# Kernel optimization log

Measured on AMD Instinct MI355X. Metric: run time of the kernel, lower is better.

## Reference

```python
import jax, jax.numpy as jnp
import numpy as np
import math

TOP_K = 2
CAP_FACTOR = 1.25
AUX_W = 0.01


def setup_inputs() -> dict:
    key = jax.random.key(0)
    k1, k2 = jax.random.split(key)
    x = jax.random.normal(k1, (8192, 4096), dtype=jnp.float32)
    # gate weight, torch init std=0.01, stored as (E, D) like nn.Linear
    gate_w = jax.random.normal(k2, (64, 4096), dtype=jnp.float32) * 0.01
    return {"x": x, "gate_w": gate_w}


def reference(x, gate_w):
    N, D = x.shape
    E = gate_w.shape[0]
    K = TOP_K
    C = max(math.ceil(CAP_FACTOR * N / E), 1)  # expert capacity

    logits = x @ gate_w.T                      # (N, E)
    probs = jax.nn.softmax(logits, axis=-1)    # (N, E)
    vals, idx = jax.lax.top_k(probs, K)        # (N, K)
    vals = vals / vals.sum(axis=-1, keepdims=True)

    # Parallel replacement of the serial double loop: flatten (N,K) row-major
    # (token-major, then k) which matches the loop iteration order exactly.
    flat_e = idx.reshape(-1)                               # (N*K,) expert ids
    oh = jax.nn.one_hot(flat_e, E, dtype=jnp.int32)        # (N*K, E)
    # exclusive prefix count of prior assignments to each expert
    pos = jnp.cumsum(oh, axis=0) - oh                      # (N*K, E)
    slot = jnp.take_along_axis(pos, flat_e[:, None], axis=1)[:, 0]  # (N*K,)
    # In the torch loop the counter saturates at C (only incremented when
    # c < C), so slot==prior_total is equivalent: kept iff prior_total < C.
    keep = slot < C
    slot_s = jnp.where(keep, slot, 0)
    tok = jnp.arange(N * K) // K

    combine_weights = jnp.zeros((N, E, C), dtype=x.dtype).at[
        tok, flat_e, slot_s].add(jnp.where(keep, vals.reshape(-1), 0.0))
    dispatch_mask = (jnp.zeros((N, E, C), dtype=jnp.int32).at[
        tok, flat_e, slot_s].add(keep.astype(jnp.int32))) > 0

    # load balancing loss
    f = oh.astype(jnp.float32).reshape(N, K, E).mean(axis=(0, 1))  # (E,)
    p = probs.mean(axis=0)                                         # (E,)
    load_loss = AUX_W * E * jnp.sum(f * p)

    return dispatch_mask, combine_weights, probs, load_loss
```

## Files before the change

### kernel.cpp

```cpp
#include <hip/hip_runtime.h>
#include <math.h>

#define N_TOK 8192
#define DIM   4096
#define NEXP  64
#define CAP   160
#define OFF_CW    (83886080ULL)
#define OFF_PROBS (167772160ULL)
#define OFF_LOSS  (168296448ULL)
#define NA    16384
#define SPLIT 8

typedef float vfloat4 __attribute__((ext_vector_type(4)));

__device__ __forceinline__ float wave_max64(float v) {
    for (int m = 1; m < 64; m <<= 1) v = fmaxf(v, __shfl_xor(v, m, 64));
    return v;
}
__device__ __forceinline__ float wave_sum64(float v) {
    for (int m = 1; m < 64; m <<= 1) v += __shfl_xor(v, m, 64);
    return v;
}
__device__ __forceinline__ void wave_argmax64(float& v, int& i) {
    for (int m = 1; m < 64; m <<= 1) {
        float ov = __shfl_xor(v, m, 64);
        int   oi = __shfl_xor(i, m, 64);
        if (ov > v || (ov == v && oi < i)) { v = ov; i = oi; }
    }
}

__global__ __launch_bounds__(256) void k_gemm_zero(const float* __restrict__ x,
                                                   const float* __restrict__ gw,
                                                   float* __restrict__ part,
                                                   float* __restrict__ out) {
    __shared__ float xs[64][68];
    __shared__ float wsh[64][68];
    const int tb = (blockIdx.x & 127) * 64;
    const int sy = blockIdx.x >> 7;
    const int d_begin = sy * (DIM / SPLIT);
    const int t  = threadIdx.x;
    const int tx = t & 15, ty = t >> 4;
    float* zbase = out + (size_t)blockIdx.x * 163840;
    const vfloat4 z = {0.f, 0.f, 0.f, 0.f};
    float acc[4][4] = {};
    for (int ci = 0; ci < (DIM / SPLIT) / 64; ++ci) {
        const int d0 = d_begin + ci * 64;
        for (int it = 0; it < 4; ++it) {
            int idx = t + 256 * it;
            int row = idx >> 4;
            int d4  = idx & 15;
            *(float4*)(&xs[row][4 * d4]) =
                *(const float4*)(x + (size_t)(tb + row) * DIM + d0 + 4 * d4);
            *(float4*)(&wsh[row][4 * d4]) =
                *(const float4*)(gw + (size_t)row * DIM + d0 + 4 * d4);
        }
        #pragma unroll
        for (int zi = 0; zi < 5; ++zi)
            __builtin_nontemporal_store(
                z, (vfloat4*)(zbase + 4 * ((ci * 5 + zi) * 256 + t)));
        __syncthreads();
        for (int d4 = 0; d4 < 16; ++d4) {
            float4 xa[4], wb[4];
            for (int i = 0; i < 4; ++i) xa[i] = *(const float4*)(&xs[ty + 16 * i][4 * d4]);
            for (int j = 0; j < 4; ++j) wb[j] = *(const float4*)(&wsh[tx + 16 * j][4 * d4]);
            for (int i = 0; i < 4; ++i)
                for (int j = 0; j < 4; ++j) {
                    acc[i][j] = fmaf(xa[i].x, wb[j].x, acc[i][j]);
                    acc[i][j] = fmaf(xa[i].y, wb[j].y, acc[i][j]);
                    acc[i][j] = fmaf(xa[i].z, wb[j].z, acc[i][j]);
                    acc[i][j] = fmaf(xa[i].w, wb[j].w, acc[i][j]);
                }
        }
        __syncthreads();
    }
    for (int i = 0; i < 4; ++i)
        for (int j = 0; j < 4; ++j)
            part[(size_t)sy * N_TOK * NEXP +
                 (size_t)(tb + ty + 16 * i) * NEXP + (tx + 16 * j)] = acc[i][j];
}

__global__ __launch_bounds__(256) void k_router(const float* __restrict__ part,
                                                float* __restrict__ probs_out,
                                                int* __restrict__ rec_e,
                                                float* __restrict__ rec_w) {
    const int tok  = blockIdx.x * 4 + (threadIdx.x >> 6);
    const int lane = threadIdx.x & 63;
    float l = 0.f;
    for (int s = 0; s < SPLIT; ++s)
        l += part[(size_t)s * N_TOK * NEXP + (size_t)tok * NEXP + lane];
    const float m  = wave_max64(l);
    const float ex = expf(l - m);
    const float sm = wave_sum64(ex);
    const float p  = ex / sm;
    probs_out[(size_t)tok * NEXP + lane] = p;
    float v1 = p; int i1 = lane;
    wave_argmax64(v1, i1);
    float v2 = (lane == i1) ? -1.f : p; int i2 = lane;
    wave_argmax64(v2, i2);
    if (lane == 0) {
        const float denom = v1 + v2;
        rec_e[2 * tok]     = i1;
        rec_e[2 * tok + 1] = i2;
        rec_w[2 * tok]     = v1 / denom;
        rec_w[2 * tok + 1] = v2 / denom;
    }
}

__global__ __launch_bounds__(256) void k_preduce(const float* __restrict__ probs,
                                                 float* __restrict__ psum_part) {
    __shared__ float sh[256];
    const int e = threadIdx.x & 63, tg = threadIdx.x >> 6;
    const int tok0 = blockIdx.x * 128;
    float a = 0.f;
    for (int k = 0; k < 32; ++k)
        a += probs[(size_t)(tok0 + tg + 4 * k) * NEXP + e];
    sh[threadIdx.x] = a;
    __syncthreads();
    if (threadIdx.x < 64)
        psum_part[blockIdx.x * 64 + threadIdx.x] =
            sh[threadIdx.x] + sh[64 + threadIdx.x] +
            sh[128 + threadIdx.x] + sh[192 + threadIdx.x];
}

__global__ __launch_bounds__(256) void k_assign_scatter(const int* __restrict__ rec_e,
                                                        const float* __restrict__ rec_w,
                                                        const float* __restrict__ psum_part,
                                                        float* __restrict__ out) {
    if (blockIdx.x == 16) {
        __shared__ int hcnt[64];
        if (threadIdx.x < 64) hcnt[threadIdx.x] = 0;
        __syncthreads();
        for (int j = 0; j < 64; ++j) {
            const int e = rec_e[j * 256 + threadIdx.x];
            atomicAdd(&hcnt[e], 1);
        }
        __syncthreads();
        if (threadIdx.x < 64) {
            const int e = threadIdx.x;
            float ps = 0.f;
            for (int b = 0; b < 64; ++b) ps += psum_part[b * 64 + e];
            float term = ((float)hcnt[e] / (float)NA) * (ps / (float)N_TOK);
            term = wave_sum64(term);
            if (e == 0) out[OFF_LOSS] = 0.01f * 64.f * term;
        }
        return;
    }
    const int w    = blockIdx.x * 4 + (threadIdx.x >> 6);
    const int lane = threadIdx.x & 63;
    int base = 0;
    const unsigned long long ltmask = (1ull << lane) - 1ull;
    #pragma unroll 4
    for (int c = 0; c < NA / 64; ++c) {
        const int i = c * 64 + lane;
        const int e = rec_e[i];
        const unsigned long long mask = __ballot(e == w);
        if (e == w) {
            const int slot = base + __popcll(mask & ltmask);
            if (slot < CAP) {
                const int tok = i >> 1;
                const size_t off = (size_t)tok * (NEXP * CAP) + (size_t)w * CAP + slot;
                out[off]          = 1.0f;
                out[OFF_CW + off] = rec_w[i];
            }
        }
        base += __popcll(mask);
    }
}

extern "C" void kernel_launch(void* const* d_in, const int* in_sizes, int n_in,
                              void* d_out, int out_size, void* d_ws, size_t ws_size,
                              hipStream_t stream) {
    const float* x  = (const float*)d_in[0];
    const float* gw = (const float*)d_in[1];
    float* out = (float*)d_out;

    char* w = (char*)d_ws;
    float* part      = (float*)w;
    int*   rec_e     = (int*)(w + (size_t)SPLIT * N_TOK * NEXP * 4);
    float* rec_w     = (float*)((char*)rec_e + NA * 4);
    float* psum_part = (float*)((char*)rec_w + NA * 4);

    k_gemm_zero<<<1024, 256, 0, stream>>>(x, gw, part, out);
    k_router<<<2048, 256, 0, stream>>>(part, out + OFF_PROBS, rec_e, rec_w);
    k_preduce<<<64, 256, 0, stream>>>(out + OFF_PROBS, psum_part);
    k_assign_scatter<<<17, 256, 0, stream>>>(rec_e, rec_w, psum_part, out);
}
```

Measured before the change: 763.2 us.

## Compute gate GEMM one token per lane with scalar-broadcast weights

Replaces the LDS-tiled 64x64 gate GEMM with a scheme where each lane owns one token and keeps 64 expert accumulators in registers. The weight slice is wave-uniform, so it can be read as broadcast/scalar loads. This removes shared memory staging and barriers. The grid shrinks from 1024 to 256 blocks, with each block zeroing four times as much output, so occupancy is lower and the per-lane x reads are strided across rows rather than coalesced. That could limit how well the dominant output zero-fill stores keep the memory system busy.

```diff
diff --git a/kernel.cpp b/kernel.cpp
--- a/kernel.cpp
+++ b/kernel.cpp
@@ -10,6 +10,9 @@
 #define OFF_LOSS  (168296448ULL)
 #define NA    16384
 #define SPLIT 8
+#define DSLICE (DIM / SPLIT)
+#define DC    16
+#define NCHUNK (DSLICE / DC)
 
 typedef float vfloat4 __attribute__((ext_vector_type(4)));
 
@@ -33,50 +36,56 @@
                                                    const float* __restrict__ gw,
                                                    float* __restrict__ part,
                                                    float* __restrict__ out) {
-    __shared__ float xs[64][68];
-    __shared__ float wsh[64][68];
-    const int tb = (blockIdx.x & 127) * 64;
-    const int sy = blockIdx.x >> 7;
-    const int d_begin = sy * (DIM / SPLIT);
-    const int t  = threadIdx.x;
-    const int tx = t & 15, ty = t >> 4;
-    float* zbase = out + (size_t)blockIdx.x * 163840;
+    const int t    = threadIdx.x;
+    const int lane = t & 63;
+    const int gwid = blockIdx.x * 4 + (t >> 6);
+    const int g    = gwid & 127;
+    const int sy   = __builtin_amdgcn_readfirstlane(gwid >> 7);
+    const int tok  = g * 64 + lane;
+    const float* xrow = x  + (size_t)tok * DIM + sy * DSLICE;
+    const float* gwp  = gw + (size_t)sy * DSLICE;
+
+    float acc[64];
+    #pragma unroll
+    for (int e = 0; e < 64; ++e) acc[e] = 0.f;
+
+    float* zbase = out + (size_t)blockIdx.x * 655360;
     const vfloat4 z = {0.f, 0.f, 0.f, 0.f};
-    float acc[4][4] = {};
-    for (int ci = 0; ci < (DIM / SPLIT) / 64; ++ci) {
-        const int d0 = d_begin + ci * 64;
-        for (int it = 0; it < 4; ++it) {
-            int idx = t + 256 * it;
-            int row = idx >> 4;
-            int d4  = idx & 15;
-            *(float4*)(&xs[row][4 * d4]) =
-                *(const float4*)(x + (size_t)(tb + row) * DIM + d0 + 4 * d4);
-            *(float4*)(&wsh[row][4 * d4]) =
-                *(const float4*)(gw + (size_t)row * DIM + d0 + 4 * d4);
+
+    for (int c = 0; c < NCHUNK; ++c) {
+        float4 xv0 = *(const float4*)(xrow + c * DC +  0);
+        float4 xv1 = *(const float4*)(xrow + c * DC +  4);
+        float4 xv2 = *(const float4*)(xrow + c * DC +  8);
+        float4 xv3 = *(const float4*)(xrow + c * DC + 12);
+        #pragma unroll
+        for (int zi = 0; zi < 20; ++zi)
+            __builtin_nontemporal_store(
+                z, (vfloat4*)(zbase + 4 * ((c * 20 + zi) * 256 + t)));
+        const float* gc = gwp + c * DC;
+        #pragma unroll
+        for (int e = 0; e < 64; ++e) {
+            const float* ge = gc + (size_t)e * DIM;
+            acc[e] = fmaf(xv0.x, ge[0],  acc[e]);
+            acc[e] = fmaf(xv0.y, ge[1],  acc[e]);
+            acc[e] = fmaf(xv0.z, ge[2],  acc[e]);
+            acc[e] = fmaf(xv0.w, ge[3],  acc[e]);
+            acc[e] = fmaf(xv1.x, ge[4],  acc[e]);
+            acc[e] = fmaf(xv1.y, ge[5],  acc[e]);
+            acc[e] = fmaf(xv1.z, ge[6],  acc[e]);
+            acc[e] = fmaf(xv1.w, ge[7],  acc[e]);
+            acc[e] = fmaf(xv2.x, ge[8],  acc[e]);
+            acc[e] = fmaf(xv2.y, ge[9],  acc[e]);
+            acc[e] = fmaf(xv2.z, ge[10], acc[e]);
+            acc[e] = fmaf(xv2.w, ge[11], acc[e]);
+            acc[e] = fmaf(xv3.x, ge[12], acc[e]);
+            acc[e] = fmaf(xv3.y, ge[13], acc[e]);
+            acc[e] = fmaf(xv3.z, ge[14], acc[e]);
+            acc[e] = fmaf(xv3.w, ge[15], acc[e]);
         }
-        #pragma unroll
-        for (int zi = 0; zi < 5; ++zi)
-            __builtin_nontemporal_store(
-                z, (vfloat4*)(zbase + 4 * ((ci * 5 + zi) * 256 + t)));
-        __syncthreads();
-        for (int d4 = 0; d4 < 16; ++d4) {
-            float4 xa[4], wb[4];
-            for (int i = 0; i < 4; ++i) xa[i] = *(const float4*)(&xs[ty + 16 * i][4 * d4]);
-            for (int j = 0; j < 4; ++j) wb[j] = *(const float4*)(&wsh[tx + 16 * j][4 * d4]);
-            for (int i = 0; i < 4; ++i)
-                for (int j = 0; j < 4; ++j) {
-                    acc[i][j] = fmaf(xa[i].x, wb[j].x, acc[i][j]);
-                    acc[i][j] = fmaf(xa[i].y, wb[j].y, acc[i][j]);
-                    acc[i][j] = fmaf(xa[i].z, wb[j].z, acc[i][j]);
-                    acc[i][j] = fmaf(xa[i].w, wb[j].w, acc[i][j]);
-                }
-        }
-        __syncthreads();
     }
-    for (int i = 0; i < 4; ++i)
-        for (int j = 0; j < 4; ++j)
-            part[(size_t)sy * N_TOK * NEXP +
-                 (size_t)(tb + ty + 16 * i) * NEXP + (tx + 16 * j)] = acc[i][j];
+    float* pbase = part + ((size_t)sy * N_TOK + tok) * NEXP;
+    #pragma unroll
+    for (int e = 0; e < 64; ++e) pbase[e] = acc[e];
 }
 
 __global__ __launch_bounds__(256) void k_router(const float* __restrict__ part,
@@ -180,7 +189,7 @@
     float* rec_w     = (float*)((char*)rec_e + NA * 4);
     float* psum_part = (float*)((char*)rec_w + NA * 4);
 
-    k_gemm_zero<<<1024, 256, 0, stream>>>(x, gw, part, out);
+    k_gemm_zero<<<256, 256, 0, stream>>>(x, gw, part, out);
     k_router<<<2048, 256, 0, stream>>>(part, out + OFF_PROBS, rec_e, rec_w);
     k_preduce<<<64, 256, 0, stream>>>(out + OFF_PROBS, psum_part);
     k_assign_scatter<<<17, 256, 0, stream>>>(rec_e, rec_w, psum_part, out);
```

Result: slower. 1.495 ms (+95.8%).
